# Optimization experiments

Hardware: AMD Instinct MI355X
Metric: run time of the kernel (lower is better)

## Reference

```python
import jax, jax.numpy as jnp
import numpy as np

NB_NODE = 100000
FT = 256
OUT_FT = 256
NB_REL = 4
BATCH = 8192
DEG = 16  # padded neighbors per (node, relation)


def setup_inputs() -> dict:
    key = jax.random.key(0)
    k1, k2, k3, k4 = jax.random.split(key, 4)
    features = jax.random.normal(k1, (NB_NODE, FT), dtype=jnp.float32)
    neighbor_idx = jax.random.randint(k2, (BATCH, NB_REL, DEG), 0, NB_NODE, dtype=jnp.int32)
    # per-relation GCN weight, scaled like xavier
    W = jax.random.normal(k3, (NB_REL, FT, OUT_FT), dtype=jnp.float32) * (1.0 / np.sqrt(FT))
    b = jnp.zeros((NB_REL, OUT_FT), dtype=jnp.float32)
    prelu_a = jnp.full((1,), 0.25, dtype=jnp.float32)  # nn.PReLU() default single param
    node_list = jax.random.randint(k4, (BATCH,), 0, NB_NODE, dtype=jnp.int32)
    return {"features": features, "neighbor_idx": neighbor_idx, "W": W, "b": b,
            "prelu_a": prelu_a, "node_list": node_list, "k": 0}


def _prelu(x, a):
    return jnp.where(x >= 0, x, a * x)


def reference(features, neighbor_idx, W, b, prelu_a, node_list, k):
    # Ragged per-relation neighbor gather + mean (vectorized form of the
    # python double loop): [B, R, D, F] -> mean over D -> [B, R, F]
    v_in = jnp.mean(features[neighbor_idx], axis=2)
    # Per-relation GCN linear + PReLU: [B, R, F] x [R, F, O] -> [B, R, O]
    h = jnp.einsum('brf,rfo->bro', v_in, W) + b[None, :, :]
    h = _prelu(h, prelu_a[0])
    # isAtt=False branch: mean over relations -> [B, O]
    return jnp.mean(h, axis=1)
```

## Files before the change

### kernel.cpp

```cpp
#include <hip/hip_runtime.h>
#include <hip/hip_bf16.h>

#define B_TOT 8192
#define FT    256
#define NREL  4
#define DEG   16

typedef __attribute__((ext_vector_type(8))) short bf16x8;
typedef __attribute__((ext_vector_type(4))) float f32x4;

static __device__ __forceinline__ unsigned short f2bf(float x) {
    union { float f; unsigned int u; } c; c.f = x;
    unsigned int u = c.u;
    u += 0x7fffu + ((u >> 16) & 1u);
    return (unsigned short)(u >> 16);
}

__global__ __launch_bounds__(256) void wtrans_k(const float* __restrict__ W,
                                                unsigned short* __restrict__ Wt) {
    int ro = blockIdx.x;
    int f  = threadIdx.x;
    int r  = ro >> 8, o = ro & 255;
    float w = W[((size_t)(r * FT + f)) * 256 + o];
    Wt[(size_t)ro * FT + f] = f2bf(w);
}

__global__ __launch_bounds__(256) void gather_mean_k(const float* __restrict__ feat,
                                                     const int* __restrict__ nidx,
                                                     unsigned short* __restrict__ v) {
    int wave = threadIdx.x >> 6;
    int lane = threadIdx.x & 63;
    int task = blockIdx.x * 4 + wave;
    int b = task >> 2, r = task & 3;
    const int* idx = nidx + ((size_t)b * NREL + r) * DEG;
    int4 i0 = *(const int4*)(idx);
    int4 i1 = *(const int4*)(idx + 4);
    int4 i2 = *(const int4*)(idx + 8);
    int4 i3 = *(const int4*)(idx + 12);
    float4 s = make_float4(0.f, 0.f, 0.f, 0.f);
#define ACC(nn) { const float4 x = ((const float4*)(feat + (size_t)(nn) * FT))[lane]; \
                  s.x += x.x; s.y += x.y; s.z += x.z; s.w += x.w; }
    ACC(i0.x) ACC(i0.y) ACC(i0.z) ACC(i0.w)
    ACC(i1.x) ACC(i1.y) ACC(i1.z) ACC(i1.w)
    ACC(i2.x) ACC(i2.y) ACC(i2.z) ACC(i2.w)
    ACC(i3.x) ACC(i3.y) ACC(i3.z) ACC(i3.w)
#undef ACC
    const float inv = 1.0f / 16.0f;
    ushort4 o;
    o.x = f2bf(s.x * inv); o.y = f2bf(s.y * inv);
    o.z = f2bf(s.z * inv); o.w = f2bf(s.w * inv);
    *(ushort4*)(v + ((size_t)r * B_TOT + b) * FT + 4 * lane) = o;
}

__global__ __launch_bounds__(256) void gemm_k(const unsigned short* __restrict__ v,
                                              const unsigned short* __restrict__ Wt,
                                              const float* __restrict__ bias,
                                              const float* __restrict__ prelu,
                                              float* __restrict__ out) {
    __shared__ unsigned short As[64][264];
    __shared__ unsigned short Bs[64][264];
    int tid  = threadIdx.x;
    int lane = tid & 63, w = tid >> 6;
    int wm = w >> 1, wn = w & 1;
    int mrow = lane & 15, quad = lane >> 4;
    int m0 = blockIdx.x * 64, n0 = blockIdx.y * 64;
    float pa = prelu[0];

    f32x4 accO[2][2] = {};
    int ocol0 = n0 + wn * 32 + mrow;

    for (int r = 0; r < NREL; ++r) {
        const unsigned short* Ag = v  + ((size_t)r * B_TOT + m0) * FT;
        const unsigned short* Bg = Wt + ((size_t)r * 256  + n0) * FT;
#pragma unroll
        for (int i = 0; i < 8; ++i) {
            int u = tid + i * 256;
            int row = u >> 5, c8 = (u & 31) * 8;
            *(int4*)(&As[row][c8]) = *(const int4*)(Ag + row * FT + c8);
            *(int4*)(&Bs[row][c8]) = *(const int4*)(Bg + row * FT + c8);
        }
        __syncthreads();

        f32x4 acc[2][2] = {};
#pragma unroll
        for (int kk = 0; kk < 8; ++kk) {
            int k0 = kk * 32 + quad * 8;
            bf16x8 a0 = *(const bf16x8*)&As[wm * 32 + mrow][k0];
            bf16x8 a1 = *(const bf16x8*)&As[wm * 32 + 16 + mrow][k0];
            bf16x8 b0 = *(const bf16x8*)&Bs[wn * 32 + mrow][k0];
            bf16x8 b1 = *(const bf16x8*)&Bs[wn * 32 + 16 + mrow][k0];
            acc[0][0] = __builtin_amdgcn_mfma_f32_16x16x32_bf16(a0, b0, acc[0][0], 0, 0, 0);
            acc[1][0] = __builtin_amdgcn_mfma_f32_16x16x32_bf16(a1, b0, acc[1][0], 0, 0, 0);
            acc[0][1] = __builtin_amdgcn_mfma_f32_16x16x32_bf16(a0, b1, acc[0][1], 0, 0, 0);
            acc[1][1] = __builtin_amdgcn_mfma_f32_16x16x32_bf16(a1, b1, acc[1][1], 0, 0, 0);
        }
        __syncthreads();

        float b0v = bias[r * 256 + ocol0];
        float b1v = bias[r * 256 + ocol0 + 16];
#pragma unroll
        for (int mt = 0; mt < 2; ++mt)
#pragma unroll
            for (int i = 0; i < 4; ++i) {
                float h0 = acc[mt][0][i] + b0v; h0 = (h0 >= 0.f) ? h0 : pa * h0;
                float h1 = acc[mt][1][i] + b1v; h1 = (h1 >= 0.f) ? h1 : pa * h1;
                accO[mt][0][i] += h0;
                accO[mt][1][i] += h1;
            }
    }

#pragma unroll
    for (int mt = 0; mt < 2; ++mt)
#pragma unroll
        for (int i = 0; i < 4; ++i) {
            int row = m0 + wm * 32 + mt * 16 + quad * 4 + i;
            out[(size_t)row * 256 + ocol0]      = accO[mt][0][i] * 0.25f;
            out[(size_t)row * 256 + ocol0 + 16] = accO[mt][1][i] * 0.25f;
        }
}

extern "C" void kernel_launch(void* const* d_in, const int* in_sizes, int n_in,
                              void* d_out, int out_size, void* d_ws, size_t ws_size,
                              hipStream_t stream) {
    const float* feat  = (const float*)d_in[0];
    const int*   nidx  = (const int*)  d_in[1];
    const float* W     = (const float*)d_in[2];
    const float* bias  = (const float*)d_in[3];
    const float* prelu = (const float*)d_in[4];
    float* out = (float*)d_out;

    unsigned short* v  = (unsigned short*)d_ws;
    unsigned short* Wt = v + (size_t)NREL * B_TOT * FT;

    wtrans_k<<<NREL * 256, 256, 0, stream>>>(W, Wt);
    gather_mean_k<<<B_TOT, 256, 0, stream>>>(feat, nidx, v);
    gemm_k<<<dim3(B_TOT / 64, 256 / 64), 256, 0, stream>>>(v, Wt, bias, prelu, out);
}
```

Baseline: 225.1 us.

## Convert features to bf16 before gathering and tile the weight transpose

Adds a pass that converts the full feature table to bf16 in the workspace, then gathers and averages the bf16 rows, halving the bytes moved by the random-row gather. The weight transpose is rewritten to use a padded shared-memory tile so both its reads and writes are coalesced. The conversion pass reads the whole table every call, which adds fixed traffic, and the gathered features are now rounded to bf16 before summing. It falls back to the old fp32 gather if the workspace is too small.

```diff
diff --git a/kernel.cpp b/kernel.cpp
--- a/kernel.cpp
+++ b/kernel.cpp
@@ -15,14 +15,68 @@
     u += 0x7fffu + ((u >> 16) & 1u);
     return (unsigned short)(u >> 16);
 }
+static __device__ __forceinline__ float bf2f(unsigned short h) {
+    union { unsigned int u; float f; } c; c.u = ((unsigned int)h) << 16;
+    return c.f;
+}
+
+__global__ __launch_bounds__(256) void cvt_feat_k(const float* __restrict__ f,
+                                                  unsigned short* __restrict__ fb,
+                                                  int n4) {
+    int i = blockIdx.x * 256 + threadIdx.x;
+    if (i < n4) {
+        float4 x = ((const float4*)f)[i];
+        ushort4 o;
+        o.x = f2bf(x.x); o.y = f2bf(x.y); o.z = f2bf(x.z); o.w = f2bf(x.w);
+        ((ushort4*)fb)[i] = o;
+    }
+}
 
 __global__ __launch_bounds__(256) void wtrans_k(const float* __restrict__ W,
                                                 unsigned short* __restrict__ Wt) {
-    int ro = blockIdx.x;
-    int f  = threadIdx.x;
-    int r  = ro >> 8, o = ro & 255;
-    float w = W[((size_t)(r * FT + f)) * 256 + o];
-    Wt[(size_t)ro * FT + f] = f2bf(w);
+    __shared__ float t[64][65];
+    int r = blockIdx.z, ft = blockIdx.y, ot = blockIdx.x;
+    int c = threadIdx.x & 63, rw = threadIdx.x >> 6;
+    const float* src = W + ((size_t)r * 256 + ft * 64) * 256 + ot * 64;
+#pragma unroll
+    for (int i = 0; i < 16; ++i) {
+        int row = i * 4 + rw;
+        t[row][c] = src[(size_t)row * 256 + c];
+    }
+    __syncthreads();
+    unsigned short* dst = Wt + ((size_t)r * 256 + ot * 64) * 256 + ft * 64;
+#pragma unroll
+    for (int i = 0; i < 16; ++i) {
+        int row = i * 4 + rw;
+        dst[(size_t)row * 256 + c] = f2bf(t[c][row]);
+    }
+}
+
+__global__ __launch_bounds__(256) void gather_mean_bf16_k(const unsigned short* __restrict__ fb,
+                                                          const int* __restrict__ nidx,
+                                                          unsigned short* __restrict__ v) {
+    int wave = threadIdx.x >> 6;
+    int lane = threadIdx.x & 63;
+    int task = blockIdx.x * 4 + wave;
+    int b = task >> 2, r = task & 3;
+    const int* idx = nidx + ((size_t)b * NREL + r) * DEG;
+    int4 i0 = *(const int4*)(idx);
+    int4 i1 = *(const int4*)(idx + 4);
+    int4 i2 = *(const int4*)(idx + 8);
+    int4 i3 = *(const int4*)(idx + 12);
+    float s0 = 0.f, s1 = 0.f, s2 = 0.f, s3 = 0.f;
+#define ACC(nn) { const ushort4 x = ((const ushort4*)(fb + (size_t)(nn) * FT))[lane]; \
+                  s0 += bf2f(x.x); s1 += bf2f(x.y); s2 += bf2f(x.z); s3 += bf2f(x.w); }
+    ACC(i0.x) ACC(i0.y) ACC(i0.z) ACC(i0.w)
+    ACC(i1.x) ACC(i1.y) ACC(i1.z) ACC(i1.w)
+    ACC(i2.x) ACC(i2.y) ACC(i2.z) ACC(i2.w)
+    ACC(i3.x) ACC(i3.y) ACC(i3.z) ACC(i3.w)
+#undef ACC
+    const float inv = 1.0f / 16.0f;
+    ushort4 o;
+    o.x = f2bf(s0 * inv); o.y = f2bf(s1 * inv);
+    o.z = f2bf(s2 * inv); o.w = f2bf(s3 * inv);
+    *(ushort4*)(v + ((size_t)r * B_TOT + b) * FT + 4 * lane) = o;
 }
 
 __global__ __launch_bounds__(256) void gather_mean_k(const float* __restrict__ feat,
@@ -129,10 +183,25 @@
     const float* prelu = (const float*)d_in[4];
     float* out = (float*)d_out;
 
-    unsigned short* v  = (unsigned short*)d_ws;
-    unsigned short* Wt = v + (size_t)NREL * B_TOT * FT;
-
-    wtrans_k<<<NREL * 256, 256, 0, stream>>>(W, Wt);
-    gather_mean_k<<<B_TOT, 256, 0, stream>>>(feat, nidx, v);
-    gemm_k<<<dim3(B_TOT / 64, 256 / 64), 256, 0, stream>>>(v, Wt, bias, prelu, out);
-}
+    const size_t feat_elems = (size_t)in_sizes[0];
+    const size_t fb_bytes = feat_elems * 2;
+    const size_t v_bytes  = (size_t)NREL * B_TOT * FT * 2;
+    const size_t wt_bytes = (size_t)NREL * 256 * FT * 2;
+
+    if (ws_size >= fb_bytes + v_bytes + wt_bytes) {
+        unsigned short* fb = (unsigned short*)d_ws;
+        unsigned short* v  = fb + feat_elems;
+        unsigned short* Wt = v + (size_t)NREL * B_TOT * FT;
+        int n4 = (int)(feat_elems / 4);
+        cvt_feat_k<<<(n4 + 255) / 256, 256, 0, stream>>>(feat, fb, n4);
+        wtrans_k<<<dim3(4, 4, 4), 256, 0, stream>>>(W, Wt);
+        gather_mean_bf16_k<<<B_TOT, 256, 0, stream>>>(fb, nidx, v);
+        gemm_k<<<dim3(B_TOT / 64, 256 / 64), 256, 0, stream>>>(v, Wt, bias, prelu, out);
+    } else {
+        unsigned short* v  = (unsigned short*)d_ws;
+        unsigned short* Wt = v + (size_t)NREL * B_TOT * FT;
+        wtrans_k<<<dim3(4, 4, 4), 256, 0, stream>>>(W, Wt);
+        gather_mean_k<<<B_TOT, 256, 0, stream>>>(feat, nidx, v);
+        gemm_k<<<dim3(B_TOT / 64, 256 / 64), 256, 0, stream>>>(v, Wt, bias, prelu, out);
+    }
+}
```

After: 213.3 us. 5.2% less time.
